# Kernel tuning notes

Hardware: AMD Instinct MI355X
Metric: run time of the kernel (lower is better)

## Reference

```python
import jax, jax.numpy as jnp
import numpy as np

B, N, DIM = 2, 1024, 512
HEADS, DIM_HEAD = 8, 64
HIDDEN = HEADS * DIM_HEAD
TIME_DIM = 512
BIAS_DIM = 16
EPS = 1e-5


def setup_inputs() -> dict:
    key = jax.random.key(0)
    ks = jax.random.split(key, 12)
    inp = {
        "x": jax.random.normal(ks[0], (B, N, DIM), jnp.float32),
        "residx": jnp.broadcast_to(jnp.arange(N, dtype=jnp.float32), (B, N)),
        "time": jax.random.normal(ks[1], (B, 1, TIME_DIM), jnp.float32),
        "attn_bias": jax.random.normal(ks[2], (B, BIAS_DIM, N, N), jnp.float32),
        "seq_mask": jnp.ones((B, N), jnp.float32),
        # params
        "gamma": jnp.ones((DIM,), jnp.float32),
        "Wt": jax.random.normal(ks[3], (2 * DIM, TIME_DIM), jnp.float32) * 0.02,
        "bt": jax.random.normal(ks[4], (2 * DIM,), jnp.float32) * 0.02,
        "Wb": jax.random.normal(ks[5], (HEADS, BIAS_DIM), jnp.float32) * 0.1,
        "bb": jax.random.normal(ks[6], (HEADS,), jnp.float32) * 0.1,
        "Wq": jax.random.normal(ks[7], (HIDDEN, DIM), jnp.float32) * (DIM ** -0.5),
        "Wkv": jax.random.normal(ks[8], (2 * HIDDEN, DIM), jnp.float32) * (DIM ** -0.5),
        "Wo": jax.random.normal(ks[9], (DIM, HIDDEN), jnp.float32) * (HIDDEN ** -0.5),
    }
    return inp


def _layer_norm(x, gamma):
    mu = jnp.mean(x, axis=-1, keepdims=True)
    var = jnp.var(x, axis=-1, keepdims=True)
    return (x - mu) * jax.lax.rsqrt(var + EPS) * gamma  # beta buffer is zeros


def reference(x, residx, time, attn_bias, seq_mask, gamma, Wt, bt, Wb, bb, Wq, Wkv, Wo):
    h, d = HEADS, DIM_HEAD
    b, n, _ = x.shape
    xn = _layer_norm(x, gamma)
    # time conditioning: SiLU -> Linear -> chunk into scale/shift
    t = jax.nn.silu(time) @ Wt.T + bt  # [B,1,2*dim]
    scale, shift = jnp.split(t, 2, axis=-1)
    xn = xn * (scale + 1.0) + shift
    xn = xn * seq_mask[..., None]
    # projections
    q = (xn @ Wq.T).reshape(b, n, h, d).transpose(0, 2, 1, 3)  # b h n d
    kv = xn @ Wkv.T
    k_, v_ = jnp.split(kv, 2, axis=-1)
    k = k_.reshape(b, n, h, d).transpose(0, 2, 1, 3)
    v = v_.reshape(b, n, h, d).transpose(0, 2, 1, 3)
    q = q * (d ** -0.5)
    sim = jnp.einsum('bhid,bhjd->bhij', q, k)
    # attn bias projection: b a i j -> linear over a -> b h i j
    bias = jnp.einsum('baij,ha->bhij', attn_bias, Wb) + bb[None, :, None, None]
    sim = sim + bias
    # mask
    attn_mask = seq_mask[:, None, :, None] * seq_mask[:, None, None, :]  # b 1 i j
    sim = sim - (1.0 - attn_mask) * 1e6
    attn = jax.nn.softmax(sim, axis=-1)
    out = jnp.einsum('bhij,bhjd->bhid', attn, v)
    out = out.transpose(0, 2, 1, 3).reshape(b, n, h * d)
    out = out @ Wo.T
    out = out * seq_mask[..., None]
    return out
```

## Files before the change

kernel.cpp:

```cpp
#include <hip/hip_runtime.h>
#include <cstdint>
#include <cstddef>

typedef __bf16 bf16x8 __attribute__((ext_vector_type(8)));
typedef float f32x4 __attribute__((ext_vector_type(4)));
typedef unsigned short u16;
typedef unsigned short u16x8 __attribute__((ext_vector_type(8)));

__device__ __forceinline__ u16 f2b(float f) {
    union { float f; uint32_t u; } v; v.f = f;
    uint32_t r = v.u + 0x7fffu + ((v.u >> 16) & 1u);
    return (u16)(r >> 16);
}
__device__ __forceinline__ float b2f(u16 h) {
    union { uint32_t u; float f; } v; v.u = ((uint32_t)h) << 16; return v.f;
}

__global__ __launch_bounds__(256) void prep_kernel(
    const float* __restrict__ Wq, const float* __restrict__ Wkv, const float* __restrict__ Wo,
    const float* __restrict__ timep, const float* __restrict__ Wt, const float* __restrict__ bt,
    u16* __restrict__ wqkv, u16* __restrict__ wo, float* __restrict__ tbuf)
{
    __shared__ float st[512];
    int bx = blockIdx.x, tid = threadIdx.x;
    if (bx < 1024) {
        int i = bx * 256 + tid;
        float4 v; u16* dp;
        if (i < 65536)      { v = ((const float4*)Wq)[i];            dp = wqkv + (size_t)i * 4; }
        else if (i < 196608){ int k = i - 65536;  v = ((const float4*)Wkv)[k]; dp = wqkv + 262144 + (size_t)k * 4; }
        else                { int k = i - 196608; v = ((const float4*)Wo)[k];  dp = wo + (size_t)k * 4; }
        ushort4 o;
        o.x = f2b(v.x); o.y = f2b(v.y); o.z = f2b(v.z); o.w = f2b(v.w);
        *(ushort4*)dp = o;
    } else {
        int bx2 = bx - 1024;
        int b = bx2 >> 2, ch = bx2 & 3;
        for (int k = tid; k < 512; k += 256) {
            float v = timep[b * 512 + k];
            st[k] = v / (1.f + __expf(-v));
        }
        __syncthreads();
        int o = ch * 256 + tid;
        const float4* wrow = (const float4*)(Wt + (size_t)o * 512);
        float acc = bt[o];
        #pragma unroll 4
        for (int k4 = 0; k4 < 128; k4++) {
            float4 w = wrow[k4];
            acc += st[k4*4+0]*w.x + st[k4*4+1]*w.y + st[k4*4+2]*w.z + st[k4*4+3]*w.w;
        }
        tbuf[b * 1024 + o] = acc;
    }
}

__global__ __launch_bounds__(64) void ln_cond_kernel(
    const float* __restrict__ x, const float* __restrict__ gamma,
    const float* __restrict__ tbuf, const float* __restrict__ seq_mask,
    u16* __restrict__ xn)
{
    int m = blockIdx.x;
    int b = m >> 10;
    int lane = threadIdx.x;
    const float* xr = x + (size_t)m * 512;
    int c0 = lane * 8;
    float4 v0 = *(const float4*)(xr + c0);
    float4 v1 = *(const float4*)(xr + c0 + 4);
    float xv[8] = {v0.x, v0.y, v0.z, v0.w, v1.x, v1.y, v1.z, v1.w};
    float s = 0.f, ss = 0.f;
    #pragma unroll
    for (int e = 0; e < 8; e++) { s += xv[e]; ss += xv[e]*xv[e]; }
    #pragma unroll
    for (int off = 1; off < 64; off <<= 1) {
        s  += __shfl_xor(s, off);
        ss += __shfl_xor(ss, off);
    }
    float mu = s * (1.f/512.f);
    float var = ss * (1.f/512.f) - mu*mu;
    float rs = rsqrtf(var + 1e-5f);
    float mk = seq_mask[m];
    u16x8 ov;
    #pragma unroll
    for (int e = 0; e < 8; e++) {
        int c = c0 + e;
        float sc = tbuf[b*1024 + c] + 1.f;
        float sh = tbuf[b*1024 + 512 + c];
        float val = ((xv[e] - mu) * rs * gamma[c] * sc + sh) * mk;
        ov[e] = f2b(val);
    }
    *(u16x8*)&xn[(size_t)m * 512 + c0] = ov;
}

#define TSP 258
__global__ __launch_bounds__(256) void qkv_bias_kernel(
    const float* __restrict__ ab, const float* __restrict__ Wb, const float* __restrict__ bbv,
    const u16* __restrict__ xn, const u16* __restrict__ wqkv,
    u16* __restrict__ bias_t, u16* __restrict__ qb, u16* __restrict__ kb, u16* __restrict__ vT)
{
    __shared__ u16 SH[10240];
    __shared__ float wbs[128];
    __shared__ float bbs[8];
    const int tid = threadIdx.x;
    const int bx = blockIdx.x;
    if (bx >= 192) {
        if (tid < 128) wbs[tid] = Wb[tid];
        if (tid < 8) bbs[tid] = bbv[tid];
        __syncthreads();
        int bx2 = bx - 192;
        int b = bx2 >> 10;
        int rem = bx2 & 1023;
        int i4 = rem >> 2, jt4 = rem & 3;
        int row_l = tid >> 6, chunk = tid & 63;
        int i = i4*4 + row_l;
        int j = jt4*256 + chunk*4;
        const float* base = ab + ((size_t)b << 24) + ((size_t)i << 10) + j;

        f32x4 v[16];
        #pragma unroll
        for (int a = 0; a < 16; a++)
            v[a] = *(const f32x4*)(base + ((size_t)a << 20));
        f32x4 acc[8];
        #pragma unroll
        for (int h = 0; h < 8; h++) {
            float bv = bbs[h];
            acc[h][0] = bv; acc[h][1] = bv; acc[h][2] = bv; acc[h][3] = bv;
        }
        #pragma unroll
        for (int a = 0; a < 16; a++)
            #pragma unroll
            for (int h = 0; h < 8; h++)
                acc[h] += wbs[h*16 + a] * v[a];
        #pragma unroll
        for (int h = 0; h < 8; h++) {
            ushort4 o;
            o.x = f2b(acc[h][0]); o.y = f2b(acc[h][1]); o.z = f2b(acc[h][2]); o.w = f2b(acc[h][3]);
            *(ushort4*)&SH[(h*4 + row_l)*TSP + chunk*4] = o;
        }
        __syncthreads();
        int hh = tid >> 5;
        int rest = tid & 31;
        int li = rest & 15, shalf = rest >> 4;
        int it32 = i4 >> 3, isub = (i4 >> 2) & 1, g = i4 & 3;
        #pragma unroll
        for (int ss = 0; ss < 2; ss++) {
            int jtsub = shalf*2 + ss;
            int jt = jt4*4 + jtsub;
            u16 tmp[16];
            #pragma unroll
            for (int r = 0; r < 4; r++)
                #pragma unroll
                for (int fj = 0; fj < 4; fj++)
                    tmp[r*4 + fj] = SH[(hh*4 + r)*TSP + jtsub*64 + fj*16 + li];
            size_t tb = ((((size_t)(b*8 + hh))*32 + it32)*16 + jt)*2048 + (size_t)(isub*64 + g*16 + li)*16;
            *(uint4*)&bias_t[tb]     = *(uint4*)&tmp[0];
            *(uint4*)&bias_t[tb + 8] = *(uint4*)&tmp[8];
        }
    } else {
        u16 (*As)[40] = (u16(*)[40])&SH[0];
        u16 (*Bs)[40] = (u16(*)[40])&SH[5120];
        int v = bx;
        const int m0 = (v & 15) * 128, n0 = (v >> 4) * 128;
        const int lane = tid & 63, wid = tid >> 6;
        const int wr = wid >> 1, wc = wid & 1;
        const int li = lane & 15, g = lane >> 4;
        f32x4 acc[4][4] = {};
        const int srow = tid >> 2, scol = (tid & 3) * 8;
        for (int k0 = 0; k0 < 512; k0 += 32) {
            *(bf16x8*)&As[srow][scol]      = *(const bf16x8*)&xn[(size_t)(m0+srow)*512 + k0 + scol];
            *(bf16x8*)&As[srow+64][scol]   = *(const bf16x8*)&xn[(size_t)(m0+srow+64)*512 + k0 + scol];
            *(bf16x8*)&Bs[srow][scol]      = *(const bf16x8*)&wqkv[(size_t)(n0+srow)*512 + k0 + scol];
            *(bf16x8*)&Bs[srow+64][scol]   = *(const bf16x8*)&wqkv[(size_t)(n0+srow+64)*512 + k0 + scol];
            __syncthreads();
            bf16x8 a[4], bf[4];
            #pragma unroll
            for (int mi = 0; mi < 4; mi++) a[mi]  = *(const bf16x8*)&As[wr*64 + mi*16 + li][g*8];
            #pragma unroll
            for (int nj = 0; nj < 4; nj++) bf[nj] = *(const bf16x8*)&Bs[wc*64 + nj*16 + li][g*8];
            #pragma unroll
            for (int mi = 0; mi < 4; mi++)
                #pragma unroll
                for (int nj = 0; nj < 4; nj++)
                    acc[mi][nj] = __builtin_amdgcn_mfma_f32_16x16x32_bf16(a[mi], bf[nj], acc[mi][nj], 0, 0, 0);
            __syncthreads();
        }
        #pragma unroll
        for (int mi = 0; mi < 4; mi++)
            #pragma unroll
            for (int nj = 0; nj < 4; nj++) {
                int o = n0 + wc*64 + nj*16 + li;
                int m_base = m0 + wr*64 + mi*16 + g*4;
                if (o < 1024) {
                    #pragma unroll
                    for (int r = 0; r < 4; r++) {
                        int m = m_base + r;
                        int b = m >> 10, n = m & 1023;
                        float vv = acc[mi][nj][r];
                        if (o < 512) {
                            qb[((size_t)(b*8 + (o>>6))*1024 + n)*64 + (o&63)] = f2b(vv * 0.125f);
                        } else {
                            int oo = o - 512;
                            kb[((size_t)(b*8 + (oo>>6))*1024 + n)*64 + (oo&63)] = f2b(vv);
                        }
                    }
                } else {
                    int oo = o - 1024;
                    int b = m_base >> 10, n = m_base & 1023;
                    ushort4 ov;
                    ov.x = f2b(acc[mi][nj][0]); ov.y = f2b(acc[mi][nj][1]);
                    ov.z = f2b(acc[mi][nj][2]); ov.w = f2b(acc[mi][nj][3]);
                    *(ushort4*)&vT[((size_t)(b*8 + (oo>>6))*64 + (oo&63))*1024 + n] = ov;
                }
            }
    }
}

__global__ __launch_bounds__(256) void attn_kernel(
    const u16* __restrict__ qb, const u16* __restrict__ kb, const u16* __restrict__ vT,
    const u16* __restrict__ bias_t, const float* __restrict__ seq_mask,
    float* __restrict__ Om, float* __restrict__ ml)
{
    __shared__ u16 Ks[2][4096];
    __shared__ u16 Vs[2][4096];
    __shared__ u16 Ps[4][1024];
    __shared__ float mjs[512];
    int tid = threadIdx.x;
    int lane = tid & 63, w = tid >> 6;
    int li = lane & 15, g = lane >> 4;
    int it = blockIdx.x, h = blockIdx.y;
    int bz = blockIdx.z;
    int b = bz >> 1, jh = bz & 1;
    int bh = b*8 + h;
    int i0 = it * 64;
    int jt0 = jh * 8;
    const u16* qp = qb + ((size_t)bh*1024 + i0) * 64;
    const u16* kp = kb + (size_t)bh*65536 + (size_t)jt0*4096;
    const u16* vp = vT + (size_t)bh*65536;
    const u16* bp = bias_t + (((size_t)(bh*32 + it*2 + (w>>1)))*16 + jt0)*2048 + ((w&1)*64 + lane)*16;

    if (tid < 128) ((float4*)mjs)[tid] = ((const float4*)(seq_mask + b*1024 + jh*512))[tid];

    bf16x8 aq0 = *(const bf16x8*)&qp[(w*16 + li)*64 + g*8];
    bf16x8 aq1 = *(const bf16x8*)&qp[(w*16 + li)*64 + 32 + g*8];

    const int sli = tid & 15, sg = (tid >> 4) & 3, sf = tid >> 6;
    const int kslot0 = (sf*128 + sg*16 + sli) * 8;
    bf16x8 kr0, kr1, vr0, vr1, bfA_c, bfB_c, bfA_n, bfB_n;
    #define LOADT(jx) do { \
        kr0 = *(const bf16x8*)&kp[(size_t)(jx)*4096 + (sf*16 + sli)*64 + sg*8]; \
        kr1 = *(const bf16x8*)&kp[(size_t)(jx)*4096 + (sf*16 + sli)*64 + 32 + sg*8]; \
        vr0 = *(const bf16x8*)&vp[(size_t)(sf*16 + sli)*1024 + (jt0+(jx))*64 + sg*8]; \
        vr1 = *(const bf16x8*)&vp[(size_t)(sf*16 + sli)*1024 + (jt0+(jx))*64 + 32 + sg*8]; \
        bfA_n = *(const bf16x8*)&bp[(size_t)(jx)*2048]; \
        bfB_n = *(const bf16x8*)&bp[(size_t)(jx)*2048 + 8]; \
    } while (0)
    #define STORET(buf_) do { \
        *(bf16x8*)&Ks[buf_][kslot0]       = kr0; \
        *(bf16x8*)&Ks[buf_][kslot0 + 512] = kr1; \
        *(bf16x8*)&Vs[buf_][kslot0]       = vr0; \
        *(bf16x8*)&Vs[buf_][kslot0 + 512] = vr1; \
    } while (0)

    f32x4 oacc[4] = {};
    float m_run[4], l_run[4], mi[4];
    #pragma unroll
    for (int r = 0; r < 4; r++) {
        m_run[r] = -3e38f; l_run[r] = 0.f;
        mi[r] = seq_mask[b*1024 + i0 + w*16 + g*4 + r];
    }

    LOADT(0); STORET(0); bfA_c = bfA_n; bfB_c = bfB_n;
    __syncthreads();

    for (int jtt = 0; jtt < 8; jtt++) {
        int cur = jtt & 1;
        if (jtt < 7) LOADT(jtt + 1);
        f32x4 s[4] = {};
        #pragma unroll
        for (int fj = 0; fj < 4; fj++) {
            bf16x8 bk0 = *(const bf16x8*)&Ks[cur][(fj*128 + g*16 + li)*8];
            bf16x8 bk1 = *(const bf16x8*)&Ks[cur][(fj*128 + g*16 + li)*8 + 512];
            s[fj] = __builtin_amdgcn_mfma_f32_16x16x32_bf16(aq0, bk0, s[fj], 0, 0, 0);
            s[fj] = __builtin_amdgcn_mfma_f32_16x16x32_bf16(aq1, bk1, s[fj], 0, 0, 0);
        }
        float pmax[4] = {-3e38f, -3e38f, -3e38f, -3e38f};
        #pragma unroll
        for (int fj = 0; fj < 4; fj++) {
            float mj = mjs[jtt*64 + fj*16 + li];
            #pragma unroll
            for (int r = 0; r < 4; r++) {
                float bvl = (r < 2) ? b2f(((u16x8)bfA_c)[r*4 + fj]) : b2f(((u16x8)bfB_c)[(r-2)*4 + fj]);
                float sv = s[fj][r] + bvl;
                sv -= (1.f - mi[r]*mj) * 1e6f;
                s[fj][r] = sv;
                pmax[r] = fmaxf(pmax[r], sv);
            }
        }
        #pragma unroll
        for (int r = 0; r < 4; r++)
            #pragma unroll
            for (int off = 1; off < 16; off <<= 1)
                pmax[r] = fmaxf(pmax[r], __shfl_xor(pmax[r], off));
        float alpha[4], psum[4] = {0.f, 0.f, 0.f, 0.f}, mnew[4];
        #pragma unroll
        for (int r = 0; r < 4; r++) {
            mnew[r] = fmaxf(m_run[r], pmax[r]);
            alpha[r] = __expf(m_run[r] - mnew[r]);
            m_run[r] = mnew[r];
        }
        #pragma unroll
        for (int fj = 0; fj < 4; fj++)
            #pragma unroll
            for (int r = 0; r < 4; r++) {
                float p = __expf(s[fj][r] - mnew[r]);
                s[fj][r] = p;
                psum[r] += p;
            }
        #pragma unroll
        for (int r = 0; r < 4; r++) {
            #pragma unroll
            for (int off = 1; off < 16; off <<= 1) psum[r] += __shfl_xor(psum[r], off);
            l_run[r] = l_run[r]*alpha[r] + psum[r];
        }
        #pragma unroll
        for (int fj = 0; fj < 4; fj++) {
            int ph2 = fj >> 1;
            int pg = (fj*2 + (li >> 3)) & 3;
            int pin = li & 7;
            #pragma unroll
            for (int r = 0; r < 4; r++)
                Ps[w][(ph2*64 + pg*16 + g*4 + r)*8 + pin] = f2b(s[fj][r]);
        }
        #pragma unroll
        for (int fd = 0; fd < 4; fd++)
            #pragma unroll
            for (int r = 0; r < 4; r++)
                oacc[fd][r] *= alpha[r];
        bf16x8 ap0 = *(const bf16x8*)&Ps[w][(g*16 + li)*8];
        bf16x8 ap1 = *(const bf16x8*)&Ps[w][(g*16 + li)*8 + 512];
        #pragma unroll
        for (int fd = 0; fd < 4; fd++) {
            bf16x8 bv0 = *(const bf16x8*)&Vs[cur][(fd*128 + g*16 + li)*8];
            bf16x8 bv1 = *(const bf16x8*)&Vs[cur][(fd*128 + g*16 + li)*8 + 512];
            oacc[fd] = __builtin_amdgcn_mfma_f32_16x16x32_bf16(ap0, bv0, oacc[fd], 0, 0, 0);
            oacc[fd] = __builtin_amdgcn_mfma_f32_16x16x32_bf16(ap1, bv1, oacc[fd], 0, 0, 0);
        }
        if (jtt < 7) { STORET(cur ^ 1); bfA_c = bfA_n; bfB_c = bfB_n; }
        __syncthreads();
    }
    size_t pbase = ((size_t)(bh*16 + it)*2 + jh) * 4096;
    #pragma unroll
    for (int fd = 0; fd < 4; fd++)
        #pragma unroll
        for (int r = 0; r < 4; r++)
            Om[pbase + (size_t)(w*16 + g*4 + r)*64 + fd*16 + li] = oacc[fd][r];
    if (li == 0) {
        #pragma unroll
        for (int r = 0; r < 4; r++) {
            size_t mb = ((size_t)(bh*16 + it)*2 + jh) * 128 + (w*16 + g*4 + r)*2;
            ml[mb] = m_run[r]; ml[mb + 1] = l_run[r];
        }
    }
    #undef LOADT
    #undef STORET
}

__global__ __launch_bounds__(256) void merge_kernel(
    const float* __restrict__ Om, const float* __restrict__ ml, u16* __restrict__ aout)
{
    int blk = blockIdx.x;
    int bh = blk >> 4, it = blk & 15;
    int b = bh >> 3, h = bh & 7;
    int tid = threadIdx.x;
    int row = tid >> 2, dc = (tid & 3) * 16;
    size_t p0 = ((size_t)blk*2 + 0)*4096 + (size_t)row*64 + dc;
    size_t p1 = ((size_t)blk*2 + 1)*4096 + (size_t)row*64 + dc;
    size_t m0i = ((size_t)blk*2 + 0)*128 + row*2;
    size_t m1i = ((size_t)blk*2 + 1)*128 + row*2;
    float m0 = ml[m0i], l0 = ml[m0i + 1];
    float m1 = ml[m1i], l1 = ml[m1i + 1];
    float mm = fmaxf(m0, m1);
    float e0 = __expf(m0 - mm), e1 = __expf(m1 - mm);
    float linv = 1.f / (l0*e0 + l1*e1);
    int i = it*64 + row;
    u16* op = &aout[((size_t)(b*1024 + i))*512 + h*64 + dc];
    #pragma unroll
    for (int c4 = 0; c4 < 4; c4++) {
        f32x4 v0 = *(const f32x4*)&Om[p0 + c4*4];
        f32x4 v1 = *(const f32x4*)&Om[p1 + c4*4];
        ushort4 o;
        o.x = f2b((v0[0]*e0 + v1[0]*e1)*linv);
        o.y = f2b((v0[1]*e0 + v1[1]*e1)*linv);
        o.z = f2b((v0[2]*e0 + v1[2]*e1)*linv);
        o.w = f2b((v0[3]*e0 + v1[3]*e1)*linv);
        *(ushort4*)&op[c4*4] = o;
    }
}

__global__ __launch_bounds__(256) void out_gemm_kernel(
    const u16* __restrict__ aout, const u16* __restrict__ wo,
    const float* __restrict__ seq_mask, float* __restrict__ out)
{
    __shared__ u16 As[64][40];
    __shared__ u16 Bs[64][40];
    const int tid = threadIdx.x;
    const int lane = tid & 63, wid = tid >> 6;
    const int wr = wid >> 1, wc = wid & 1;
    const int li = lane & 15, g = lane >> 4;
    const int m0 = blockIdx.x * 64, n0 = blockIdx.y * 64;

    f32x4 acc[2][2] = {};
    const int lrow = tid >> 2, lcol = (tid & 3) * 8;
    for (int k0 = 0; k0 < 512; k0 += 32) {
        *(bf16x8*)&As[lrow][lcol] = *(const bf16x8*)&aout[(size_t)(m0+lrow)*512 + k0 + lcol];
        *(bf16x8*)&Bs[lrow][lcol] = *(const bf16x8*)&wo[(size_t)(n0+lrow)*512 + k0 + lcol];
        __syncthreads();
        bf16x8 a[2], bf[2];
        #pragma unroll
        for (int fi = 0; fi < 2; fi++) a[fi]  = *(const bf16x8*)&As[wr*32 + fi*16 + li][g*8];
        #pragma unroll
        for (int fj = 0; fj < 2; fj++) bf[fj] = *(const bf16x8*)&Bs[wc*32 + fj*16 + li][g*8];
        #pragma unroll
        for (int fi = 0; fi < 2; fi++)
            #pragma unroll
            for (int fj = 0; fj < 2; fj++)
                acc[fi][fj] = __builtin_amdgcn_mfma_f32_16x16x32_bf16(a[fi], bf[fj], acc[fi][fj], 0, 0, 0);
        __syncthreads();
    }
    #pragma unroll
    for (int fi = 0; fi < 2; fi++)
        #pragma unroll
        for (int fj = 0; fj < 2; fj++)
            #pragma unroll
            for (int r = 0; r < 4; r++) {
                int m = m0 + wr*32 + fi*16 + g*4 + r;
                int o = n0 + wc*32 + fj*16 + li;
                out[(size_t)m*512 + o] = acc[fi][fj][r] * seq_mask[m];
            }
}

extern "C" void kernel_launch(void* const* d_in, const int* in_sizes, int n_in,
                              void* d_out, int out_size, void* d_ws, size_t ws_size,
                              hipStream_t stream) {
    const float* x         = (const float*)d_in[0];
    const float* timep     = (const float*)d_in[2];
    const float* attn_bias = (const float*)d_in[3];
    const float* seq_mask  = (const float*)d_in[4];
    const float* gamma     = (const float*)d_in[5];
    const float* Wt        = (const float*)d_in[6];
    const float* bt        = (const float*)d_in[7];
    const float* Wb        = (const float*)d_in[8];
    const float* bb        = (const float*)d_in[9];
    const float* Wq        = (const float*)d_in[10];
    const float* Wkv       = (const float*)d_in[11];
    const float* Wo        = (const float*)d_in[12];
    float* out = (float*)d_out;

    char* ws = (char*)d_ws;
    size_t off = 0;
    auto alloc = [&](size_t bytes) { char* p = ws + off; off += (bytes + 255) & ~(size_t)255; return p; };
    float* tbuf  = (float*)alloc(2 * 1024 * 4);
    u16* xn      = (u16*)alloc((size_t)2048 * 512 * 2);
    u16* wqkv    = (u16*)alloc((size_t)1536 * 512 * 2);
    u16* wo      = (u16*)alloc((size_t)512 * 512 * 2);
    u16* qb      = (u16*)alloc((size_t)2 * 8 * 1024 * 64 * 2);
    u16* kb      = (u16*)alloc((size_t)2 * 8 * 1024 * 64 * 2);
    u16* vT      = (u16*)alloc((size_t)2 * 8 * 64 * 1024 * 2);
    u16* bias_t  = (u16*)alloc((size_t)2 * 8 * 1024 * 1024 * 2);
    u16* aout    = (u16*)alloc((size_t)2048 * 512 * 2);
    float* Om    = (float*)alloc((size_t)256 * 2 * 4096 * 4);
    float* ml    = (float*)alloc((size_t)256 * 2 * 128 * 4);
    (void)ws_size;

    prep_kernel<<<1032, 256, 0, stream>>>(Wq, Wkv, Wo, timep, Wt, bt, wqkv, wo, tbuf);
    ln_cond_kernel<<<2048, 64, 0, stream>>>(x, gamma, tbuf, seq_mask, xn);
    qkv_bias_kernel<<<2240, 256, 0, stream>>>(attn_bias, Wb, bb, xn, wqkv, bias_t, qb, kb, vT);
    attn_kernel<<<dim3(16, 8, 4), 256, 0, stream>>>(qb, kb, vT, bias_t, seq_mask, Om, ml);
    merge_kernel<<<256, 256, 0, stream>>>(Om, ml, aout);
    out_gemm_kernel<<<dim3(32, 8), 256, 0, stream>>>(aout, wo, seq_mask, out);
}
```

Baseline: 88.21 us.

## Widen bias-projection blocks to full rows with double-buffered channel loads

Each bias block now handles four full rows of 1024 columns instead of a 4x256 tile, with each thread covering four rows. It streams the 16 bias channels through a double-buffered register pipeline rather than loading all 16 at once. This cuts the bias block count from 2048 to 512, grows shared memory to about 72KB, and raises register use to 128 accumulators per thread. Occupancy drops, which could hurt latency hiding on this memory-bound stage, but the streaming is meant to keep loads overlapped with the FMAs.

Result: slower. 96.18 us (+9.0%).

```diff
diff --git a/kernel.cpp b/kernel.cpp
--- a/kernel.cpp
+++ b/kernel.cpp
@@ -89,13 +89,12 @@
     *(u16x8*)&xn[(size_t)m * 512 + c0] = ov;
 }
 
-#define TSP 258
 __global__ __launch_bounds__(256) void qkv_bias_kernel(
     const float* __restrict__ ab, const float* __restrict__ Wb, const float* __restrict__ bbv,
     const u16* __restrict__ xn, const u16* __restrict__ wqkv,
     u16* __restrict__ bias_t, u16* __restrict__ qb, u16* __restrict__ kb, u16* __restrict__ vT)
 {
-    __shared__ u16 SH[10240];
+    __shared__ u16 SH[36864];
     __shared__ float wbs[128];
     __shared__ float bbs[8];
     const int tid = threadIdx.x;
@@ -105,51 +104,61 @@
         if (tid < 8) bbs[tid] = bbv[tid];
         __syncthreads();
         int bx2 = bx - 192;
-        int b = bx2 >> 10;
-        int rem = bx2 & 1023;
-        int i4 = rem >> 2, jt4 = rem & 3;
-        int row_l = tid >> 6, chunk = tid & 63;
-        int i = i4*4 + row_l;
-        int j = jt4*256 + chunk*4;
-        const float* base = ab + ((size_t)b << 24) + ((size_t)i << 10) + j;
-
-        f32x4 v[16];
-        #pragma unroll
-        for (int a = 0; a < 16; a++)
-            v[a] = *(const f32x4*)(base + ((size_t)a << 20));
-        f32x4 acc[8];
+        int b = bx2 >> 8;
+        int i4 = bx2 & 255;
+        const float* pbase = ab + ((size_t)b << 24) + ((size_t)(i4*4) << 10) + tid*4;
+
+        f32x4 vbuf[2][4];
+        f32x4 acc[4][8];
+        #pragma unroll
+        for (int r = 0; r < 4; r++)
+            #pragma unroll
+            for (int h = 0; h < 8; h++) {
+                acc[r][h][0] = 0.f; acc[r][h][1] = 0.f; acc[r][h][2] = 0.f; acc[r][h][3] = 0.f;
+            }
+        #pragma unroll
+        for (int r = 0; r < 4; r++) vbuf[0][r] = *(const f32x4*)(pbase + r*1024);
+        #pragma unroll
+        for (int a = 0; a < 16; a++) {
+            if (a < 15) {
+                const float* pn = pbase + ((size_t)(a + 1) << 20);
+                #pragma unroll
+                for (int r = 0; r < 4; r++) vbuf[(a+1)&1][r] = *(const f32x4*)(pn + r*1024);
+            }
+            float wa[8];
+            #pragma unroll
+            for (int h = 0; h < 8; h++) wa[h] = wbs[h*16 + a];
+            #pragma unroll
+            for (int r = 0; r < 4; r++)
+                #pragma unroll
+                for (int h = 0; h < 8; h++)
+                    acc[r][h] += wa[h] * vbuf[a&1][r];
+        }
+        int jt_w = tid >> 4, jc_w = (tid & 15) * 4;
         #pragma unroll
         for (int h = 0; h < 8; h++) {
             float bv = bbs[h];
-            acc[h][0] = bv; acc[h][1] = bv; acc[h][2] = bv; acc[h][3] = bv;
-        }
-        #pragma unroll
-        for (int a = 0; a < 16; a++)
-            #pragma unroll
-            for (int h = 0; h < 8; h++)
-                acc[h] += wbs[h*16 + a] * v[a];
+            #pragma unroll
+            for (int r = 0; r < 4; r++) {
+                ushort4 o;
+                o.x = f2b(acc[r][h][0] + bv); o.y = f2b(acc[r][h][1] + bv);
+                o.z = f2b(acc[r][h][2] + bv); o.w = f2b(acc[r][h][3] + bv);
+                *(ushort4*)&SH[(h*4 + r)*1152 + jt_w*72 + jc_w] = o;
+            }
+        }
+        __syncthreads();
+        int li = tid & 15, jt = tid >> 4;
+        int it32 = i4 >> 3, isub = (i4 >> 2) & 1, g = i4 & 3;
+        int slot = isub*64 + g*16 + li;
         #pragma unroll
         for (int h = 0; h < 8; h++) {
-            ushort4 o;
-            o.x = f2b(acc[h][0]); o.y = f2b(acc[h][1]); o.z = f2b(acc[h][2]); o.w = f2b(acc[h][3]);
-            *(ushort4*)&SH[(h*4 + row_l)*TSP + chunk*4] = o;
-        }
-        __syncthreads();
-        int hh = tid >> 5;
-        int rest = tid & 31;
-        int li = rest & 15, shalf = rest >> 4;
-        int it32 = i4 >> 3, isub = (i4 >> 2) & 1, g = i4 & 3;
-        #pragma unroll
-        for (int ss = 0; ss < 2; ss++) {
-            int jtsub = shalf*2 + ss;
-            int jt = jt4*4 + jtsub;
             u16 tmp[16];
             #pragma unroll
             for (int r = 0; r < 4; r++)
                 #pragma unroll
                 for (int fj = 0; fj < 4; fj++)
-                    tmp[r*4 + fj] = SH[(hh*4 + r)*TSP + jtsub*64 + fj*16 + li];
-            size_t tb = ((((size_t)(b*8 + hh))*32 + it32)*16 + jt)*2048 + (size_t)(isub*64 + g*16 + li)*16;
+                    tmp[r*4 + fj] = SH[(h*4 + r)*1152 + jt*72 + fj*16 + li];
+            size_t tb = ((((size_t)(b*8 + h))*32 + it32)*16 + jt)*2048 + (size_t)slot*16;
             *(uint4*)&bias_t[tb]     = *(uint4*)&tmp[0];
             *(uint4*)&bias_t[tb + 8] = *(uint4*)&tmp[8];
         }
@@ -471,7 +480,7 @@
 
     prep_kernel<<<1032, 256, 0, stream>>>(Wq, Wkv, Wo, timep, Wt, bt, wqkv, wo, tbuf);
     ln_cond_kernel<<<2048, 64, 0, stream>>>(x, gamma, tbuf, seq_mask, xn);
-    qkv_bias_kernel<<<2240, 256, 0, stream>>>(attn_bias, Wb, bb, xn, wqkv, bias_t, qb, kb, vT);
+    qkv_bias_kernel<<<704, 256, 0, stream>>>(attn_bias, Wb, bb, xn, wqkv, bias_t, qb, kb, vT);
     attn_kernel<<<dim3(16, 8, 4), 256, 0, stream>>>(qb, kb, vT, bias_t, seq_mask, Om, ml);
     merge_kernel<<<256, 256, 0, stream>>>(Om, ml, aout);
     out_gemm_kernel<<<dim3(32, 8), 256, 0, stream>>>(aout, wo, seq_mask, out);
```
